# Kernel tuning notes

Hardware: AMD Instinct MI355X
Metric: run time of the kernel (lower is better)

Reference implementation:

```python
import jax, jax.numpy as jnp
import numpy as np

HEAD_NUM = 16
QKV_DIM = 16
EMB = 256
MS_HID = 16
B, R, C = 4, 512, 512


def setup_inputs() -> dict:
    key = jax.random.key(0)
    ks = jax.random.split(key, 10)
    inv = 1.0 / np.sqrt(EMB)
    m1 = np.sqrt(0.5)
    m2 = np.sqrt(1.0 / 16.0)
    return {
        "row_emb": jax.random.normal(ks[0], (B, R, EMB), jnp.float32),
        "col_emb": jax.random.normal(ks[1], (B, C, EMB), jnp.float32),
        "cost_mat": jax.random.uniform(ks[2], (B, R, C), jnp.float32),
        # Linear(no bias) weights stored as [in, out] so y = x @ W
        "Wq": jax.random.uniform(ks[3], (EMB, HEAD_NUM * QKV_DIM), jnp.float32, -inv, inv),
        "Wk": jax.random.uniform(ks[4], (EMB, HEAD_NUM * QKV_DIM), jnp.float32, -inv, inv),
        "Wv": jax.random.uniform(ks[5], (EMB, HEAD_NUM * QKV_DIM), jnp.float32, -inv, inv),
        "mix1_weight": jax.random.uniform(ks[6], (HEAD_NUM, 2, MS_HID), jnp.float32, -m1, m1),
        "mix1_bias": jax.random.uniform(ks[7], (HEAD_NUM, MS_HID), jnp.float32, -m1, m1),
        "mix2_weight": jax.random.uniform(ks[8], (HEAD_NUM, MS_HID, 1), jnp.float32, -m2, m2),
        "mix2_bias": jax.random.uniform(ks[9], (HEAD_NUM, 1), jnp.float32, -m2, m2),
    }


def _split_heads(x):
    # [b, g, h*s] -> [b, h, g, s]
    b, g, _ = x.shape
    return x.reshape(b, g, HEAD_NUM, QKV_DIM).transpose(0, 2, 1, 3)


def reference(row_emb, col_emb, cost_mat, Wq, Wk, Wv, mix1_weight, mix1_bias, mix2_weight, mix2_bias):
    q = _split_heads(row_emb @ Wq)  # [b,h,r,s]
    k = _split_heads(col_emb @ Wk)  # [b,h,c,s]
    v = _split_heads(col_emb @ Wv)  # [b,h,c,s]

    dot = jnp.einsum("bhrs,bhcs->bhrc", q, k) / jnp.sqrt(jnp.float32(QKV_DIM))
    cost = jnp.broadcast_to(cost_mat[:, None, :, :], dot.shape)
    two = jnp.stack((dot, cost), axis=-1)  # [b,h,r,c,2]

    # per-head 2-layer MLP applied to each (row, col) score pair
    ms1 = jnp.einsum("bhrcx,hxm->bhrcm", two, mix1_weight) + mix1_bias[None, :, None, None, :]
    ms1 = jax.nn.relu(ms1)
    mixed = jnp.einsum("bhrcm,hmo->bhrco", ms1, mix2_weight)[..., 0] + mix2_bias[None, :, None, None, 0]

    weights = jax.nn.softmax(mixed, axis=3)  # [b,h,r,c]
    out = jnp.einsum("bhrc,bhcs->bhrs", weights, v)
    b, h, r, s = out.shape
    return out.transpose(0, 2, 1, 3).reshape(b, r, h * s)
```

## Files before the change

### kernel.cpp

```cpp
#include <hip/hip_runtime.h>

#define NB 4
#define NH 16
#define RR 512
#define CC 512
#define EMB 256
#define SD 16
#define MH 16

typedef __attribute__((ext_vector_type(4))) float f32x4;
typedef __fp16 half2v __attribute__((ext_vector_type(2)));
typedef __fp16 half4v __attribute__((ext_vector_type(4)));
typedef __fp16 half8v __attribute__((ext_vector_type(8)));

union H8 { half8v v; half2v h[4]; __fp16 e[8]; };
union H4 { half4v v; half2v h[2]; __fp16 e[4]; };

__global__ __launch_bounds__(256) void prep_w(
    const float* __restrict__ Wq, const float* __restrict__ Wk,
    const float* __restrict__ Wv, __fp16* __restrict__ WT) {
  int bi = blockIdx.x;
  int mat = bi >> 4, ngrp = bi & 15;
  const float* src = (mat == 0) ? Wq : (mat == 1) ? Wk : Wv;
  __fp16* dst = WT + mat * (EMB * EMB);
  int n = ngrp * 16 + (threadIdx.x >> 4);
  int e0 = (threadIdx.x & 15) * 16;
  H8 v0, v1;
#pragma unroll
  for (int j = 0; j < 8; ++j) v0.e[j] = (__fp16)src[(e0 + j) * EMB + n];
#pragma unroll
  for (int j = 0; j < 8; ++j) v1.e[j] = (__fp16)src[(e0 + 8 + j) * EMB + n];
  *(half8v*)(dst + n * EMB + e0) = v0.v;
  *(half8v*)(dst + n * EMB + e0 + 8) = v1.v;
}

__global__ __launch_bounds__(256) void proj_kernel(
    const float* __restrict__ rowe, const float* __restrict__ cole,
    const __fp16* __restrict__ WT,
    __fp16* __restrict__ Q, __fp16* __restrict__ K,
    __fp16* __restrict__ VT) {
  int tid = threadIdx.x;
  int wid = tid >> 6, lane = tid & 63, l15 = lane & 15, quad = lane >> 4;
  int wt = blockIdx.x * 4 + wid;
  int mat = wt >> 9;
  int t = wt & 511;
  int rt = t >> 2, ng = t & 3;
  const float* X = (mat == 0) ? rowe : cole;
  const __fp16* Wm = WT + mat * (EMB * EMB);
  const float* xrow = X + (size_t)(rt * 16 + l15) * EMB + quad * 8;

  half8v xf[8];
#pragma unroll
  for (int e = 0; e < 8; ++e) {
    f32x4 b0 = *(const f32x4*)(xrow + e * 32);
    f32x4 b1 = *(const f32x4*)(xrow + e * 32 + 4);
    H8 x;
    x.h[0] = __builtin_amdgcn_cvt_pkrtz(b0[0], b0[1]);
    x.h[1] = __builtin_amdgcn_cvt_pkrtz(b0[2], b0[3]);
    x.h[2] = __builtin_amdgcn_cvt_pkrtz(b1[0], b1[1]);
    x.h[3] = __builtin_amdgcn_cvt_pkrtz(b1[2], b1[3]);
    xf[e] = x.v;
  }
  int row = rt * 16 + l15;
  int b = row >> 9, loc = row & 511;
#pragma unroll
  for (int hh = 0; hh < 4; ++hh) {
    int nt = ng * 4 + hh;
    const half8v* ap = (const half8v*)(Wm + (nt * 16 + l15) * EMB + quad * 8);
    f32x4 acc = {0.f, 0.f, 0.f, 0.f};
#pragma unroll
    for (int e = 0; e < 8; ++e)
      acc = __builtin_amdgcn_mfma_f32_16x16x32_f16(ap[e * 4], xf[e], acc, 0, 0, 0);
    if (mat < 2) {
      H4 pk;
      pk.h[0] = __builtin_amdgcn_cvt_pkrtz(acc[0], acc[1]);
      pk.h[1] = __builtin_amdgcn_cvt_pkrtz(acc[2], acc[3]);
      __fp16* dst = ((mat == 0) ? Q : K) +
          ((size_t)((b * NH + nt) * 512 + loc) * SD + quad * 4);
      *(half4v*)dst = pk.v;
    } else {
#pragma unroll
      for (int i = 0; i < 4; ++i)
        VT[(size_t)((b * NH + nt) * SD + quad * 4 + i) * CC + loc] = (__fp16)acc[i];
    }
  }
}

__global__ __launch_bounds__(256) void attn_kernel(
    const __fp16* __restrict__ Q, const __fp16* __restrict__ K,
    const __fp16* __restrict__ VT, const float* __restrict__ cost,
    const float* __restrict__ m1w, const float* __restrict__ m1b,
    const float* __restrict__ m2w, const float* __restrict__ m2b,
    float* __restrict__ out) {
  __shared__ alignas(16) __fp16 Psh[4][16 * 256];
  __shared__ float Osh[2][256];
  __shared__ float MLsh[2][2][2][16];
  int tid = threadIdx.x;
  int wid = tid >> 6, lane = tid & 63, l15 = lane & 15, quad = lane >> 4;
  int rt = wid >> 1, ch = wid & 1;
  int rb = blockIdx.x, h = blockIdx.y, b = blockIdx.z;
  int bh = b * NH + h;
  int r0 = rb * 32 + rt * 16;
  int cbase = ch * 256;

  half2v wa2[8], wc2[8], wd2[8], we2[8];
#pragma unroll
  for (int mp = 0; mp < 8; ++mp) {
    wa2[mp] = half2v{(__fp16)(m1w[(h * 2 + 0) * MH + 2 * mp] * 0.25f),
                     (__fp16)(m1w[(h * 2 + 0) * MH + 2 * mp + 1] * 0.25f)};
    wc2[mp] = half2v{(__fp16)m1w[(h * 2 + 1) * MH + 2 * mp],
                     (__fp16)m1w[(h * 2 + 1) * MH + 2 * mp + 1]};
    wd2[mp] = half2v{(__fp16)m1b[h * MH + 2 * mp],
                     (__fp16)m1b[h * MH + 2 * mp + 1]};
    we2[mp] = half2v{(__fp16)m2w[h * MH + 2 * mp],
                     (__fp16)m2w[h * MH + 2 * mp + 1]};
  }
  float wb2 = m2b[h];
  const half2v hz2 = {(__fp16)0.f, (__fp16)0.f};

  half8v qf = {0, 0, 0, 0, 0, 0, 0, 0};
  const __fp16* Qb = Q + (size_t)bh * RR * SD;
  if (quad < 2) qf = *(const half8v*)(Qb + (r0 + l15) * SD + quad * 8);

  const __fp16* Kb = K + ((size_t)bh * CC + cbase) * SD;
  const float* crow = cost + ((size_t)b * RR + r0 + l15) * CC + cbase;
  __fp16* psrow = &Psh[wid][l15 * 256];

  float mrun = -1e30f;
  half8v kf_c = *(const half8v*)(Kb + l15 * SD + quad * 8);
  f32x4 cf_c = *(const f32x4*)(crow + quad * 4);
#pragma unroll 4
  for (int it = 0; it < 16; ++it) {
    int itn = (it + 1) & 15;
    half8v kf_n = *(const half8v*)(Kb + (itn * 16 + l15) * SD + quad * 8);
    f32x4 cf_n = *(const f32x4*)(crow + itn * 16 + quad * 4);

    f32x4 acc = {0.f, 0.f, 0.f, 0.f};
    acc = __builtin_amdgcn_mfma_f32_16x16x32_f16(kf_c, qf, acc, 0, 0, 0);
    int c0 = it * 16 + quad * 4;
    float sv[4];
#pragma unroll
    for (int i = 0; i < 4; ++i) {
      half2v x2 = __builtin_amdgcn_cvt_pkrtz(acc[i], acc[i]);
      half2v c2 = __builtin_amdgcn_cvt_pkrtz(cf_c[i], cf_c[i]);
      float s = wb2;
#pragma unroll
      for (int mp = 0; mp < 8; ++mp) {
        half2v t1 = __builtin_elementwise_fma(wc2[mp], c2, wd2[mp]);
        t1 = __builtin_elementwise_fma(wa2[mp], x2, t1);
        t1 = __builtin_elementwise_max(t1, hz2);
        s = __builtin_amdgcn_fdot2(we2[mp], t1, s, false);
      }
      sv[i] = s;
      mrun = fmaxf(mrun, s);
    }
    H4 pk;
    pk.h[0] = __builtin_amdgcn_cvt_pkrtz(sv[0], sv[1]);
    pk.h[1] = __builtin_amdgcn_cvt_pkrtz(sv[2], sv[3]);
    int g = ((c0 >> 3) ^ (l15 & 7));
    *(half4v*)(psrow + g * 8 + (c0 & 7)) = pk.v;
    kf_c = kf_n; cf_c = cf_n;
  }
  mrun = fmaxf(mrun, __shfl_xor(mrun, 16));
  mrun = fmaxf(mrun, __shfl_xor(mrun, 32));

  const __fp16* vb = VT + ((size_t)bh * SD + l15) * CC + cbase;
  f32x4 o = {0.f, 0.f, 0.f, 0.f};
  float lsum = 0.f;
  const float L2E = 1.44269504088896f;
  float mb2 = mrun * L2E;
  half8v vf_c = *(const half8v*)(vb + quad * 8);
  int g0 = ((quad * 8) >> 3) ^ (l15 & 7);
  H8 pr_c; pr_c.v = *(const half8v*)(psrow + g0 * 8);
#pragma unroll
  for (int it = 0; it < 8; ++it) {
    int itn = (it + 1) & 7;
    half8v vf_n = *(const half8v*)(vb + itn * 32 + quad * 8);
    int c0n = itn * 32 + quad * 8;
    int gn = ((c0n >> 3) ^ (l15 & 7));
    H8 pr_n; pr_n.v = *(const half8v*)(psrow + gn * 8);
    float p[8];
#pragma unroll
    for (int j = 0; j < 8; ++j) {
      float x = (float)pr_c.e[j];
      p[j] = __builtin_amdgcn_exp2f(fmaf(x, L2E, -mb2));
      lsum += p[j];
    }
    H8 pf;
#pragma unroll
    for (int jj = 0; jj < 4; ++jj)
      pf.h[jj] = __builtin_amdgcn_cvt_pkrtz(p[2 * jj], p[2 * jj + 1]);
    o = __builtin_amdgcn_mfma_f32_16x16x32_f16(pf.v, vf_c, o, 0, 0, 0);
    vf_c = vf_n; pr_c = pr_n;
  }
  lsum += __shfl_xor(lsum, 16);
  lsum += __shfl_xor(lsum, 32);

  if (quad == 0) { MLsh[rt][ch][0][l15] = mrun; MLsh[rt][ch][1][l15] = lsum; }
  if (ch == 1) {
#pragma unroll
    for (int i = 0; i < 4; ++i) Osh[rt][(quad * 4 + i) * 16 + l15] = o[i];
  }
  __syncthreads();
  if (ch == 0) {
#pragma unroll
    for (int i = 0; i < 4; ++i) {
      int r = quad * 4 + i;
      float m0 = MLsh[rt][0][0][r], l0 = MLsh[rt][0][1][r];
      float m1 = MLsh[rt][1][0][r], l1 = MLsh[rt][1][1][r];
      float M = fmaxf(m0, m1);
      float a0 = __builtin_amdgcn_exp2f((m0 - M) * L2E);
      float a1 = __builtin_amdgcn_exp2f((m1 - M) * L2E);
      float l = a0 * l0 + a1 * l1;
      float val = (a0 * o[i] + a1 * Osh[rt][r * 16 + l15]) / l;
      out[((size_t)b * RR + r0 + r) * (NH * SD) + h * SD + l15] = val;
    }
  }
}

extern "C" void kernel_launch(void* const* d_in, const int* in_sizes, int n_in,
                              void* d_out, int out_size, void* d_ws, size_t ws_size,
                              hipStream_t stream) {
  const float* rowe = (const float*)d_in[0];
  const float* cole = (const float*)d_in[1];
  const float* cost = (const float*)d_in[2];
  const float* Wq   = (const float*)d_in[3];
  const float* Wk   = (const float*)d_in[4];
  const float* Wv   = (const float*)d_in[5];
  const float* m1w  = (const float*)d_in[6];
  const float* m1b  = (const float*)d_in[7];
  const float* m2w  = (const float*)d_in[8];
  const float* m2b  = (const float*)d_in[9];
  float* outp = (float*)d_out;

  __fp16* ws = (__fp16*)d_ws;
  __fp16* Qw  = ws;
  __fp16* Kw  = ws + 524288;
  __fp16* VTw = ws + 1048576;
  __fp16* WTw = ws + 1572864;

  prep_w<<<dim3(48, 1, 1), 256, 0, stream>>>(Wq, Wk, Wv, WTw);
  proj_kernel<<<dim3(384, 1, 1), 256, 0, stream>>>(rowe, cole, WTw, Qw, Kw, VTw);
  attn_kernel<<<dim3(16, NH, NB), 256, 0, stream>>>(Qw, Kw, VTw, cost,
                                                    m1w, m1b, m2w, m2b, outp);
}
```

Baseline: 117.6 us.

## Split attention columns across four waves per 16-row block and double grid

Each attention block now covers 16 rows, with its four waves each taking a quarter of the columns (128). Before, two row tiles each had two column halves. The grid doubles to 32 row blocks, and a four-way log-sum-exp merge through shared memory combines the partial results. Per-block LDS shrinks, launch bounds request 4 blocks per CU, and the softmax row sum now uses a packed fdot2 on the fp16 probabilities. The cost is that Q and the MLP weights are loaded redundantly across more blocks and the merge step has more work.

```diff
diff --git a/kernel.cpp b/kernel.cpp
--- a/kernel.cpp
+++ b/kernel.cpp
@@ -86,22 +86,21 @@
   }
 }
 
-__global__ __launch_bounds__(256) void attn_kernel(
+__global__ __launch_bounds__(256, 4) void attn_kernel(
     const __fp16* __restrict__ Q, const __fp16* __restrict__ K,
     const __fp16* __restrict__ VT, const float* __restrict__ cost,
     const float* __restrict__ m1w, const float* __restrict__ m1b,
     const float* __restrict__ m2w, const float* __restrict__ m2b,
     float* __restrict__ out) {
-  __shared__ alignas(16) __fp16 Psh[4][16 * 256];
-  __shared__ float Osh[2][256];
-  __shared__ float MLsh[2][2][2][16];
+  __shared__ alignas(16) __fp16 Psh[4][16 * 128];
+  __shared__ float Osh[3][256];
+  __shared__ float MLsh[4][2][16];
   int tid = threadIdx.x;
   int wid = tid >> 6, lane = tid & 63, l15 = lane & 15, quad = lane >> 4;
-  int rt = wid >> 1, ch = wid & 1;
   int rb = blockIdx.x, h = blockIdx.y, b = blockIdx.z;
   int bh = b * NH + h;
-  int r0 = rb * 32 + rt * 16;
-  int cbase = ch * 256;
+  int r0 = rb * 16;
+  int cbase = wid * 128;
 
   half2v wa2[8], wc2[8], wd2[8], we2[8];
 #pragma unroll
@@ -117,6 +116,7 @@
   }
   float wb2 = m2b[h];
   const half2v hz2 = {(__fp16)0.f, (__fp16)0.f};
+  const half2v one2 = {(__fp16)1.f, (__fp16)1.f};
 
   half8v qf = {0, 0, 0, 0, 0, 0, 0, 0};
   const __fp16* Qb = Q + (size_t)bh * RR * SD;
@@ -124,14 +124,14 @@
 
   const __fp16* Kb = K + ((size_t)bh * CC + cbase) * SD;
   const float* crow = cost + ((size_t)b * RR + r0 + l15) * CC + cbase;
-  __fp16* psrow = &Psh[wid][l15 * 256];
+  __fp16* psrow = &Psh[wid][l15 * 128];
 
   float mrun = -1e30f;
   half8v kf_c = *(const half8v*)(Kb + l15 * SD + quad * 8);
   f32x4 cf_c = *(const f32x4*)(crow + quad * 4);
 #pragma unroll 4
-  for (int it = 0; it < 16; ++it) {
-    int itn = (it + 1) & 15;
+  for (int it = 0; it < 8; ++it) {
+    int itn = (it + 1) & 7;
     half8v kf_n = *(const half8v*)(Kb + (itn * 16 + l15) * SD + quad * 8);
     f32x4 cf_n = *(const f32x4*)(crow + itn * 16 + quad * 4);
 
@@ -173,8 +173,8 @@
   int g0 = ((quad * 8) >> 3) ^ (l15 & 7);
   H8 pr_c; pr_c.v = *(const half8v*)(psrow + g0 * 8);
 #pragma unroll
-  for (int it = 0; it < 8; ++it) {
-    int itn = (it + 1) & 7;
+  for (int it = 0; it < 4; ++it) {
+    int itn = (it + 1) & 3;
     half8v vf_n = *(const half8v*)(vb + itn * 32 + quad * 8);
     int c0n = itn * 32 + quad * 8;
     int gn = ((c0n >> 3) ^ (l15 & 7));
@@ -184,36 +184,41 @@
     for (int j = 0; j < 8; ++j) {
       float x = (float)pr_c.e[j];
       p[j] = __builtin_amdgcn_exp2f(fmaf(x, L2E, -mb2));
-      lsum += p[j];
     }
     H8 pf;
 #pragma unroll
-    for (int jj = 0; jj < 4; ++jj)
+    for (int jj = 0; jj < 4; ++jj) {
       pf.h[jj] = __builtin_amdgcn_cvt_pkrtz(p[2 * jj], p[2 * jj + 1]);
+      lsum = __builtin_amdgcn_fdot2(pf.h[jj], one2, lsum, false);
+    }
     o = __builtin_amdgcn_mfma_f32_16x16x32_f16(pf.v, vf_c, o, 0, 0, 0);
     vf_c = vf_n; pr_c = pr_n;
   }
   lsum += __shfl_xor(lsum, 16);
   lsum += __shfl_xor(lsum, 32);
 
-  if (quad == 0) { MLsh[rt][ch][0][l15] = mrun; MLsh[rt][ch][1][l15] = lsum; }
-  if (ch == 1) {
-#pragma unroll
-    for (int i = 0; i < 4; ++i) Osh[rt][(quad * 4 + i) * 16 + l15] = o[i];
+  if (quad == 0) { MLsh[wid][0][l15] = mrun; MLsh[wid][1][l15] = lsum; }
+  if (wid != 0) {
+#pragma unroll
+    for (int i = 0; i < 4; ++i) Osh[wid - 1][(quad * 4 + i) * 16 + l15] = o[i];
   }
   __syncthreads();
-  if (ch == 0) {
+  if (wid == 0) {
 #pragma unroll
     for (int i = 0; i < 4; ++i) {
       int r = quad * 4 + i;
-      float m0 = MLsh[rt][0][0][r], l0 = MLsh[rt][0][1][r];
-      float m1 = MLsh[rt][1][0][r], l1 = MLsh[rt][1][1][r];
-      float M = fmaxf(m0, m1);
+      float m0 = MLsh[0][0][r], m1 = MLsh[1][0][r];
+      float m2 = MLsh[2][0][r], m3 = MLsh[3][0][r];
+      float M = fmaxf(fmaxf(m0, m1), fmaxf(m2, m3));
       float a0 = __builtin_amdgcn_exp2f((m0 - M) * L2E);
       float a1 = __builtin_amdgcn_exp2f((m1 - M) * L2E);
-      float l = a0 * l0 + a1 * l1;
-      float val = (a0 * o[i] + a1 * Osh[rt][r * 16 + l15]) / l;
-      out[((size_t)b * RR + r0 + r) * (NH * SD) + h * SD + l15] = val;
+      float a2 = __builtin_amdgcn_exp2f((m2 - M) * L2E);
+      float a3 = __builtin_amdgcn_exp2f((m3 - M) * L2E);
+      float l = a0 * MLsh[0][1][r] + a1 * MLsh[1][1][r] +
+                a2 * MLsh[2][1][r] + a3 * MLsh[3][1][r];
+      float num = a0 * o[i] + a1 * Osh[0][r * 16 + l15] +
+                  a2 * Osh[1][r * 16 + l15] + a3 * Osh[2][r * 16 + l15];
+      out[((size_t)b * RR + r0 + r) * (NH * SD) + h * SD + l15] = num / l;
     }
   }
 }
@@ -241,6 +246,6 @@
 
   prep_w<<<dim3(48, 1, 1), 256, 0, stream>>>(Wq, Wk, Wv, WTw);
   proj_kernel<<<dim3(384, 1, 1), 256, 0, stream>>>(rowe, cole, WTw, Qw, Kw, VTw);
-  attn_kernel<<<dim3(16, NH, NB), 256, 0, stream>>>(Qw, Kw, VTw, cost,
+  attn_kernel<<<dim3(32, NH, NB), 256, 0, stream>>>(Qw, Kw, VTw, cost,
                                                     m1w, m1b, m2w, m2b, outp);
 }
```

New measurement: 118.0 us. About the same (+0.4%).
